# Kernel optimization log

Hardware: AMD Instinct MI355X
Metric: run time of the kernel (lower is better)

Reference implementation:

```python
import math
import jax, jax.numpy as jnp
import numpy as np

B, N, E, H, DPOS = 64, 196, 768, 16, 3
DH = E // H


def rel_pos(num_patches):
    # deterministic relative-position encodings [N, N, 3] = (dx, dy, d^2)
    v = int(math.isqrt(num_patches))
    ind = jnp.arange(v)[None, :] - jnp.arange(v)[:, None]          # [v, v]
    indx = jnp.tile(ind, (v, v))                                    # [N, N]
    indy = jnp.repeat(jnp.repeat(ind, v, axis=0), v, axis=1)       # [N, N]
    indd = indx ** 2 + indy ** 2
    return jnp.stack([indx, indy, indd], axis=-1).astype(jnp.float32)


def setup_inputs() -> dict:
    key = jax.random.key(0)
    ks = jax.random.split(key, 9)
    std = 0.02  # trunc_normal std used by the module's init
    return {
        "q": jax.random.normal(ks[0], (B, N, E), jnp.float32),
        "k": jax.random.normal(ks[1], (B, N, E), jnp.float32),
        "v": jax.random.normal(ks[2], (B, N, E), jnp.float32),
        "mask": jnp.ones((B, 1, N, N), jnp.bool_),
        "Wq": jax.random.normal(ks[3], (E, E), jnp.float32) * std,
        "Wk": jax.random.normal(ks[4], (E, E), jnp.float32) * std,
        "Wv": jax.random.normal(ks[5], (E, E), jnp.float32) * std,
        "Wo": jax.random.normal(ks[6], (E, E), jnp.float32) * std,
        "bo": jnp.zeros((E,), jnp.float32),
        "Wpos": jax.random.normal(ks[7], (H, DPOS), jnp.float32) * std,
        "bpos": jnp.zeros((H,), jnp.float32),
        "gating": jnp.ones((H,), jnp.float32),
    }


def reference(q, k, v, mask, Wq, Wk, Wv, Wo, bo, Wpos, bpos, gating):
    b, n, _ = q.shape

    def heads(x, W):  # [b, n, E] -> [b, H, n, DH]
        return (x @ W.T).reshape(b, n, H, DH).transpose(0, 2, 1, 3)

    Q, K, V = heads(q, Wq), heads(k, Wk), heads(v, Wv)

    energy = jnp.einsum('bhqd,bhkd->bhqk', Q, K) / math.sqrt(DH)
    energy = jnp.where(mask, energy, -jnp.inf)
    content = jax.nn.softmax(energy, axis=-1)                      # [b, H, n, n]

    rel = rel_pos(n)                                               # [n, n, 3]
    pos = jnp.einsum('qkp,hp->hqk', rel, Wpos) + bpos[:, None, None]
    pos = jax.nn.softmax(pos, axis=-1)[None]                       # [1, H, n, n]

    g = jax.nn.sigmoid(gating)[None, :, None, None]
    score = (1.0 - g) * content + g * pos
    score = score / jnp.sum(score, axis=-1, keepdims=True)

    attn = jnp.einsum('bhqk,bhkd->bhqd', score, V)
    out = attn.transpose(0, 2, 1, 3).reshape(b, n, E) @ Wo.T + bo
    return out
```

## Files before the change

### kernel.cpp

```cpp
#include <hip/hip_runtime.h>
#include <hip/hip_bf16.h>

#define BB 64
#define NN 196
#define EE 768
#define HH 16
#define DHH 48

typedef short bf16x8 __attribute__((ext_vector_type(8)));
typedef float f32x4 __attribute__((ext_vector_type(4)));
typedef unsigned short u16;
typedef unsigned short u16x8 __attribute__((ext_vector_type(8)));
typedef unsigned int u32;

static __device__ __forceinline__ u16 f2bf(float f) {
  union { float f; u32 u; } un; un.f = f;
  u32 u = un.u;
  u32 r = (u + 0x7fffu + ((u >> 16) & 1u)) >> 16;
  return (u16)r;
}

static __device__ __forceinline__ u16 f2bf_hw(float f) {
  __hip_bfloat16 h = __float2bfloat16(f);
  return __builtin_bit_cast(u16, h);
}

#define GLOAD16(GP, LP)                                                        \
  __builtin_amdgcn_global_load_lds(                                            \
      (const __attribute__((address_space(1))) void*)(GP),                     \
      (__attribute__((address_space(3))) void*)(LP), 16, 0, 0)

static __device__ __forceinline__ int xcd_swz(int bid, int nwg) {
  int q = nwg >> 3, r = nwg & 7;
  int xcd = bid & 7, i = bid >> 3;
  return (xcd < r ? xcd * (q + 1) : r * (q + 1) + (xcd - r) * q) + i;
}

__global__ __launch_bounds__(64) void pos_kernel(const float* __restrict__ Wpos,
                                                 const float* __restrict__ bpos,
                                                 float* __restrict__ pos) {
  int bid = blockIdx.x;
  int h = bid / NN, q = bid % NN;
  int lane = threadIdx.x;
  float w0 = Wpos[h * 3 + 0], w1 = Wpos[h * 3 + 1], w2 = Wpos[h * 3 + 2];
  float bb = bpos[h];
  int qx = q % 14, qy = q / 14;
  float e[4];
  float mx = -1e30f;
#pragma unroll
  for (int i = 0; i < 4; ++i) {
    int k = lane + 64 * i;
    float val = -1e30f;
    if (k < NN) {
      int kx = k % 14, ky = k / 14;
      float dx = (float)(kx - qx), dy = (float)(ky - qy);
      val = w0 * dx + w1 * dy + w2 * (dx * dx + dy * dy) + bb;
    }
    e[i] = val;
    mx = fmaxf(mx, val);
  }
#pragma unroll
  for (int off = 1; off < 64; off <<= 1) mx = fmaxf(mx, __shfl_xor(mx, off));
  float s = 0.f;
#pragma unroll
  for (int i = 0; i < 4; ++i) {
    int k = lane + 64 * i;
    float p = (k < NN) ? expf(e[i] - mx) : 0.f;
    e[i] = p;
    s += p;
  }
#pragma unroll
  for (int off = 1; off < 64; off <<= 1) s += __shfl_xor(s, off);
  float inv = 1.f / s;
#pragma unroll
  for (int i = 0; i < 4; ++i) {
    int k = lane + 64 * i;
    if (k < NN) pos[(size_t)h * NN * NN + (size_t)q * NN + k] = e[i] * inv;
  }
}

__global__ __launch_bounds__(256) void cvtw_kernel(const float* __restrict__ W0,
                                                   const float* __restrict__ W1,
                                                   const float* __restrict__ W2,
                                                   const float* __restrict__ W3,
                                                   u16* __restrict__ out) {
  const float* Ws[4] = {W0, W1, W2, W3};
  int mat = blockIdx.y;
  const float* src = Ws[mat];
  int idx = blockIdx.x * 256 + threadIdx.x;
  float4 f = ((const float4*)src)[idx];
  short4 s;
  s.x = (short)f2bf_hw(f.x);
  s.y = (short)f2bf_hw(f.y);
  s.z = (short)f2bf_hw(f.z);
  s.w = (short)f2bf_hw(f.w);
  *(short4*)(out + (size_t)mat * EE * EE + (size_t)idx * 4) = s;
}

__global__ __launch_bounds__(256) void cvtx_kernel(const float* __restrict__ q,
                                                   const float* __restrict__ k,
                                                   const float* __restrict__ v,
                                                   u16* __restrict__ qb,
                                                   u16* __restrict__ kb,
                                                   u16* __restrict__ vb) {
  const float* srcs[3] = {q, k, v};
  u16* dsts[3] = {qb, kb, vb};
  const float* src = srcs[blockIdx.y];
  u16* dst = dsts[blockIdx.y];
#pragma unroll
  for (int c = 0; c < 4; ++c) {
    size_t idx = (size_t)blockIdx.x * 1024 + c * 256 + threadIdx.x;
    float4 f = ((const float4*)src)[idx];
    short4 s;
    s.x = (short)f2bf_hw(f.x);
    s.y = (short)f2bf_hw(f.y);
    s.z = (short)f2bf_hw(f.z);
    s.w = (short)f2bf_hw(f.w);
    ((short4*)dst)[idx] = s;
  }
}

template <bool OUT_F32>
static __device__ __forceinline__ void gemm_body(const u16* __restrict__ Aptr,
                                                 const u16* __restrict__ Wb,
                                                 void* __restrict__ Yptr,
                                                 const float* __restrict__ bias,
                                                 int m0, int n0) {
  __shared__ u16 As[3][128 * 32];
  __shared__ u16 Bs[3][128 * 32];
  const int tid = threadIdx.x;
  const int lane = tid & 63, wid = tid >> 6;
  const int wm = wid >> 1, wn = wid & 1;
  const int r16 = lane & 15, g4 = lane >> 4;
  f32x4 acc[4][4];
#pragma unroll
  for (int i = 0; i < 4; ++i)
#pragma unroll
    for (int j = 0; j < 4; ++j) acc[i][j] = (f32x4){0.f, 0.f, 0.f, 0.f};

  auto gloadA = [&](int b, int k0) {
#pragma unroll
    for (int c = 0; c < 2; ++c) {
      int s = c * 256 + tid;
      GLOAD16(Aptr + (size_t)(m0 + (s >> 2)) * EE + k0 + (s & 3) * 8,
              &As[b][s * 8]);
    }
  };
  auto gloadB = [&](int b, int k0) {
#pragma unroll
    for (int c = 0; c < 2; ++c) {
      int s = c * 256 + tid;
      GLOAD16(Wb + (size_t)(n0 + (s >> 2)) * EE + k0 + (s & 3) * 8,
              &Bs[b][s * 8]);
    }
  };

  gloadA(0, 0);  gloadB(0, 0);
  gloadA(1, 32); gloadB(1, 32);
  asm volatile("s_waitcnt vmcnt(4)" ::: "memory");
  asm volatile("s_barrier" ::: "memory");

  for (int t = 0; t < 24; ++t) {
    const int cb = t % 3;
    const int sb = (t + 2) % 3;
    const bool st = t < 22;
    if (st) {
      gloadA(sb, (t + 2) * 32);
      gloadB(sb, (t + 2) * 32);
    }
    bf16x8 af[4], bf[4];
#pragma unroll
    for (int i = 0; i < 4; ++i)
      af[i] = *(const bf16x8*)&As[cb][(wm * 64 + i * 16 + r16) * 32 + g4 * 8];
#pragma unroll
    for (int j = 0; j < 4; ++j)
      bf[j] = *(const bf16x8*)&Bs[cb][(wn * 64 + j * 16 + r16) * 32 + g4 * 8];
#pragma unroll
    for (int i = 0; i < 4; ++i)
#pragma unroll
      for (int j = 0; j < 4; ++j)
        acc[i][j] = __builtin_amdgcn_mfma_f32_16x16x32_bf16(af[i], bf[j], acc[i][j], 0, 0, 0);
    if (st)
      asm volatile("s_waitcnt vmcnt(4)" ::: "memory");
    else
      asm volatile("s_waitcnt vmcnt(0)" ::: "memory");
    asm volatile("s_barrier" ::: "memory");
  }

#pragma unroll
  for (int i = 0; i < 4; ++i) {
    int row = m0 + wm * 64 + i * 16 + g4 * 4;
#pragma unroll
    for (int j = 0; j < 4; ++j) {
      int col = n0 + wn * 64 + j * 16 + r16;
#pragma unroll
      for (int v = 0; v < 4; ++v) {
        float val = acc[i][j][v];
        if (OUT_F32)
          ((float*)Yptr)[(size_t)(row + v) * EE + col] = val + bias[col];
        else
          ((u16*)Yptr)[(size_t)(row + v) * EE + col] = f2bf(val);
      }
    }
  }
}

__global__ __launch_bounds__(256) void qkv_gemm(const u16* __restrict__ qb,
                                                const u16* __restrict__ kb,
                                                const u16* __restrict__ vb,
                                                const u16* __restrict__ Wqb,
                                                const u16* __restrict__ Wkb,
                                                const u16* __restrict__ Wvb,
                                                u16* __restrict__ Qp,
                                                u16* __restrict__ Kp,
                                                u16* __restrict__ Vp) {
  int sid = xcd_swz(blockIdx.x, 3 * 98 * 6);
  int z = sid / 588, rem = sid % 588;
  int m0 = (rem / 6) * 128, n0 = (rem % 6) * 128;
  const u16* A = (z == 0) ? qb : (z == 1) ? kb : vb;
  const u16* W = (z == 0) ? Wqb : (z == 1) ? Wkb : Wvb;
  u16* Y = (z == 0) ? Qp : (z == 1) ? Kp : Vp;
  gemm_body<false>(A, W, Y, nullptr, m0, n0);
}

__global__ __launch_bounds__(256) void out_gemm(const u16* __restrict__ ctx,
                                                const u16* __restrict__ Wob,
                                                float* __restrict__ out,
                                                const float* __restrict__ bo) {
  int sid = xcd_swz(blockIdx.x, 98 * 6);
  int m0 = (sid / 6) * 128, n0 = (sid % 6) * 128;
  gemm_body<true>(ctx, Wob, out, bo, m0, n0);
}

__global__ __launch_bounds__(512) void attn_kernel(const u16* __restrict__ Qp,
                                                   const u16* __restrict__ Kp,
                                                   const u16* __restrict__ Vp,
                                                   const float* __restrict__ pos,
                                                   const float* __restrict__ gating,
                                                   u16* __restrict__ ctx) {
  __shared__ u16 Ks[208 * 72];
  __shared__ u16 Vt[48 * 232];
  __shared__ u16 sc[8][16 * 224];
  int bh = blockIdx.x;
  int b = bh >> 4, h = bh & 15;
  int tid = threadIdx.x;
  int wid = tid >> 6, lane = tid & 63;
  int r16 = lane & 15, g4 = lane >> 4;

  const u16* Qb = Qp + (size_t)b * NN * EE + h * DHH;
  const u16* Kb = Kp + (size_t)b * NN * EE + h * DHH;
  const u16* Vb = Vp + (size_t)b * NN * EE + h * DHH;

  bf16x8 aQ0[2], aQ1[2];
#pragma unroll
  for (int i = 0; i < 2; ++i) {
    int rt = wid + 8 * i;
    if (rt < 13) {
      int qrow = rt * 16 + r16;
      if (qrow > NN - 1) qrow = NN - 1;
      const u16* qp = Qb + (size_t)qrow * EE;
      aQ0[i] = *(const bf16x8*)(qp + g4 * 8);
      aQ1[i] = *(const bf16x8*)(qp + 32 + g4 * 8);
    }
  }

  {
    u32* z = (u32*)&Ks[0];
    for (int i = tid; i < (208 * 72) / 2; i += 512) z[i] = 0u;
    z = (u32*)&Vt[0];
    for (int i = tid; i < (48 * 232) / 2; i += 512) z[i] = 0u;
  }
  __syncthreads();
  for (int c = tid; c < NN * 12; c += 512) {
    int row = c / 12, k4 = (c % 12) * 4;
    short4 v = *(const short4*)(Kb + (size_t)row * EE + k4);
    *(short4*)&Ks[row * 72 + k4] = v;
  }
  for (int c = tid; c < NN * 12; c += 512) {
    int key = c / 12, d4 = (c % 12) * 4;
    short4 v = *(const short4*)(Vb + (size_t)key * EE + d4);
    Vt[(d4 + 0) * 232 + key] = (u16)v.x;
    Vt[(d4 + 1) * 232 + key] = (u16)v.y;
    Vt[(d4 + 2) * 232 + key] = (u16)v.z;
    Vt[(d4 + 3) * 232 + key] = (u16)v.w;
  }
  __syncthreads();

  float g = 1.f / (1.f + expf(-gating[h]));
  float omg = 1.f - g;
  u16* scw = &sc[wid][0];
  const float scale = 0.14433756729740643f;
  const float* posh = pos + (size_t)h * NN * NN;

#pragma unroll
  for (int ii = 0; ii < 2; ++ii) {
    int rt = wid + 8 * ii;
    if (rt < 13) {
      int q0 = rt * 16;
      int qg[4];
#pragma unroll
      for (int v = 0; v < 4; ++v) qg[v] = q0 + g4 * 4 + v;
      float pvv[13][4];
#pragma unroll
      for (int ct = 0; ct < 13; ++ct) {
        int cix = ct * 16 + r16;
#pragma unroll
        for (int v = 0; v < 4; ++v)
          pvv[ct][v] = (cix < NN && qg[v] < NN)
                           ? posh[(size_t)qg[v] * NN + cix] : 0.f;
      }
      f32x4 e[13];
#pragma unroll
      for (int ct = 0; ct < 13; ++ct) {
        bf16x8 b0 = *(const bf16x8*)&Ks[(ct * 16 + r16) * 72 + g4 * 8];
        bf16x8 b1 = *(const bf16x8*)&Ks[(ct * 16 + r16) * 72 + 32 + g4 * 8];
        f32x4 t = (f32x4){0.f, 0.f, 0.f, 0.f};
        t = __builtin_amdgcn_mfma_f32_16x16x32_bf16(aQ0[ii], b0, t, 0, 0, 0);
        t = __builtin_amdgcn_mfma_f32_16x16x32_bf16(aQ1[ii], b1, t, 0, 0, 0);
        e[ct] = t;
      }
      float mx[4] = {-1e30f, -1e30f, -1e30f, -1e30f};
#pragma unroll
      for (int ct = 0; ct < 13; ++ct) {
        int cix = ct * 16 + r16;
        bool valid = cix < NN;
#pragma unroll
        for (int v = 0; v < 4; ++v) {
          float ev = e[ct][v] * scale;
          ev = valid ? ev : -1e30f;
          e[ct][v] = ev;
          mx[v] = fmaxf(mx[v], ev);
        }
      }
#pragma unroll
      for (int v = 0; v < 4; ++v)
#pragma unroll
        for (int off = 1; off < 16; off <<= 1) mx[v] = fmaxf(mx[v], __shfl_xor(mx[v], off));
      float sm[4] = {0.f, 0.f, 0.f, 0.f};
#pragma unroll
      for (int ct = 0; ct < 13; ++ct)
#pragma unroll
        for (int v = 0; v < 4; ++v) {
          float p = __expf(e[ct][v] - mx[v]);
          e[ct][v] = p;
          sm[v] += p;
        }
#pragma unroll
      for (int v = 0; v < 4; ++v)
#pragma unroll
        for (int off = 1; off < 16; off <<= 1) sm[v] += __shfl_xor(sm[v], off);
      float oinv[4];
#pragma unroll
      for (int v = 0; v < 4; ++v) oinv[v] = omg / sm[v];
#pragma unroll
      for (int ct = 0; ct < 14; ++ct)
#pragma unroll
        for (int v = 0; v < 4; ++v) {
          float s = (ct < 13) ? e[ct][v] * oinv[v] + g * pvv[ct][v] : 0.f;
          scw[(g4 * 4 + v) * 224 + ct * 16 + r16] = f2bf_hw(s);
        }
      asm volatile("s_waitcnt lgkmcnt(0)" ::: "memory");
      bf16x8 aS[7];
#pragma unroll
      for (int kt = 0; kt < 7; ++kt)
        aS[kt] = *(const bf16x8*)&scw[r16 * 224 + kt * 32 + g4 * 8];
#pragma unroll
      for (int dt = 0; dt < 3; ++dt) {
        f32x4 pv = (f32x4){0.f, 0.f, 0.f, 0.f};
#pragma unroll
        for (int kt = 0; kt < 7; ++kt) {
          bf16x8 bV = *(const bf16x8*)&Vt[(dt * 16 + r16) * 232 + kt * 32 + g4 * 8];
          pv = __builtin_amdgcn_mfma_f32_16x16x32_bf16(aS[kt], bV, pv, 0, 0, 0);
        }
#pragma unroll
        for (int v = 0; v < 4; ++v) {
          if (qg[v] < NN)
            ctx[((size_t)b * NN + qg[v]) * EE + h * DHH + dt * 16 + r16] = f2bf(pv[v]);
        }
      }
    }
  }
}

extern "C" void kernel_launch(void* const* d_in, const int* in_sizes, int n_in,
                              void* d_out, int out_size, void* d_ws, size_t ws_size,
                              hipStream_t stream) {
  const float* q = (const float*)d_in[0];
  const float* k = (const float*)d_in[1];
  const float* v = (const float*)d_in[2];
  const float* Wq = (const float*)d_in[4];
  const float* Wk = (const float*)d_in[5];
  const float* Wv = (const float*)d_in[6];
  const float* Wo = (const float*)d_in[7];
  const float* bo = (const float*)d_in[8];
  const float* Wpos = (const float*)d_in[9];
  const float* bpos = (const float*)d_in[10];
  const float* gating = (const float*)d_in[11];
  float* out = (float*)d_out;

  char* ws = (char*)d_ws;
  const size_t elems = (size_t)BB * NN * EE;
  u16* Qp = (u16*)ws;
  u16* Kp = Qp + elems;
  u16* Vp = Kp + elems;
  u16* ctx = Vp + elems;
  float* pos = (float*)(ws + 4 * elems * sizeof(u16));
  u16* Wqb = (u16*)(ws + 4 * elems * sizeof(u16) + (size_t)HH * NN * NN * sizeof(float));
  u16* Wkb = Wqb + (size_t)EE * EE;
  u16* Wvb = Wkb + (size_t)EE * EE;
  u16* Wob = Wvb + (size_t)EE * EE;
  u16* qb = (u16*)d_out;
  u16* kb = qb + elems;
  u16* vb = ctx;

  hipLaunchKernelGGL(pos_kernel, dim3(HH * NN), dim3(64), 0, stream, Wpos, bpos, pos);
  hipLaunchKernelGGL(cvtw_kernel, dim3(EE * EE / 4 / 256, 4), dim3(256), 0, stream,
                     Wq, Wk, Wv, Wo, Wqb);
  hipLaunchKernelGGL(cvtx_kernel, dim3(2352, 3), dim3(256), 0, stream,
                     q, k, v, qb, kb, vb);

  hipLaunchKernelGGL(qkv_gemm, dim3(3 * 98 * 6), dim3(256), 0, stream,
                     qb, kb, vb, Wqb, Wkb, Wvb, Qp, Kp, Vp);

  hipLaunchKernelGGL(attn_kernel, dim3(BB * HH), dim3(512), 0, stream,
                     Qp, Kp, Vp, pos, gating, ctx);

  hipLaunchKernelGGL(out_gemm, dim3(98 * 6), dim3(256), 0, stream,
                     ctx, Wob, out, bo);
}
```

Baseline: 214.9 us.

## Apply positional softmax via extra MFMA with precomputed gated bf16 position matrix

The positional softmax is now prescaled by the sigmoid gate in pos_kernel and stored as a padded bf16 matrix. The attention kernel loads it directly as MFMA A-operands and adds its product with V through an extra MFMA per tile. This replaces the per-element fp32 pos gathers and the blending FMA. The content softmax also drops max-subtraction, which removes a reduction pass but risks overflow for large logits. The dead attn_kernel stub is left in the file, and launch bounds ask for two blocks per CU.

```diff
diff --git a/kernel.cpp b/kernel.cpp
--- a/kernel.cpp
+++ b/kernel.cpp
@@ -38,13 +38,24 @@
 
 __global__ __launch_bounds__(64) void pos_kernel(const float* __restrict__ Wpos,
                                                  const float* __restrict__ bpos,
-                                                 float* __restrict__ pos) {
+                                                 const float* __restrict__ gating,
+                                                 u16* __restrict__ posb) {
   int bid = blockIdx.x;
-  int h = bid / NN, q = bid % NN;
+  int h = bid / 208, qrow = bid % 208;
+  u16* dst = posb + ((size_t)h * 208 + qrow) * 224;
   int lane = threadIdx.x;
+  if (qrow >= NN) {
+#pragma unroll
+    for (int i = 0; i < 4; ++i) {
+      int k = lane + 64 * i;
+      if (k < 224) dst[k] = 0;
+    }
+    return;
+  }
   float w0 = Wpos[h * 3 + 0], w1 = Wpos[h * 3 + 1], w2 = Wpos[h * 3 + 2];
   float bb = bpos[h];
-  int qx = q % 14, qy = q / 14;
+  float g = 1.f / (1.f + expf(-gating[h]));
+  int qx = qrow % 14, qy = qrow / 14;
   float e[4];
   float mx = -1e30f;
 #pragma unroll
@@ -71,11 +82,11 @@
   }
 #pragma unroll
   for (int off = 1; off < 64; off <<= 1) s += __shfl_xor(s, off);
-  float inv = 1.f / s;
+  float ginv = g / s;
 #pragma unroll
   for (int i = 0; i < 4; ++i) {
     int k = lane + 64 * i;
-    if (k < NN) pos[(size_t)h * NN * NN + (size_t)q * NN + k] = e[i] * inv;
+    if (k < 224) dst[k] = (k < NN) ? f2bf_hw(e[i] * ginv) : (u16)0;
   }
 }
 
@@ -232,12 +243,11 @@
   gemm_body<true>(ctx, Wob, out, bo, m0, n0);
 }
 
-__global__ __launch_bounds__(512) void attn_kernel(const u16* __restrict__ Qp,
-                                                   const u16* __restrict__ Kp,
-                                                   const u16* __restrict__ Vp,
-                                                   const float* __restrict__ pos,
-                                                   const float* __restrict__ gating,
-                                                   u16* __restrict__ ctx) {
+__global__ __launch_bounds__(512, 2) void attn_kernel(const u16* __restrict__ Qp,
+                                                      const u16* __restrict__ Kp,
+                                                      const u16* __restrict__ Vp,
+                                                      const u16* __restrict__ posb,
+                                                      u16* __restrict__ ctx) {
   __shared__ u16 Ks[208 * 72];
   __shared__ u16 Vt[48 * 232];
   __shared__ u16 sc[8][16 * 224];
@@ -250,6 +260,7 @@
   const u16* Qb = Qp + (size_t)b * NN * EE + h * DHH;
   const u16* Kb = Kp + (size_t)b * NN * EE + h * DHH;
   const u16* Vb = Vp + (size_t)b * NN * EE + h * DHH;
+  const u16* ph = posb + (size_t)h * 208 * 224;
 
   bf16x8 aQ0[2], aQ1[2];
 #pragma unroll
@@ -286,11 +297,8 @@
   }
   __syncthreads();
 
-  float g = 1.f / (1.f + expf(-gating[h]));
-  float omg = 1.f - g;
   u16* scw = &sc[wid][0];
   const float scale = 0.14433756729740643f;
-  const float* posh = pos + (size_t)h * NN * NN;
 
 #pragma unroll
   for (int ii = 0; ii < 2; ++ii) {
@@ -300,15 +308,11 @@
       int qg[4];
 #pragma unroll
       for (int v = 0; v < 4; ++v) qg[v] = q0 + g4 * 4 + v;
-      float pvv[13][4];
-#pragma unroll
-      for (int ct = 0; ct < 13; ++ct) {
-        int cix = ct * 16 + r16;
-#pragma unroll
-        for (int v = 0; v < 4; ++v)
-          pvv[ct][v] = (cix < NN && qg[v] < NN)
-                           ? posh[(size_t)qg[v] * NN + cix] : 0.f;
-      }
+      bf16x8 aP[7];
+      const u16* prow = ph + (size_t)(q0 + r16) * 224;
+#pragma unroll
+      for (int kt = 0; kt < 7; ++kt)
+        aP[kt] = *(const bf16x8*)(prow + kt * 32 + g4 * 8);
       f32x4 e[13];
 #pragma unroll
       for (int ct = 0; ct < 13; ++ct) {
@@ -319,44 +323,139 @@
         t = __builtin_amdgcn_mfma_f32_16x16x32_bf16(aQ1[ii], b1, t, 0, 0, 0);
         e[ct] = t;
       }
-      float mx[4] = {-1e30f, -1e30f, -1e30f, -1e30f};
+      float sm[4] = {0.f, 0.f, 0.f, 0.f};
 #pragma unroll
       for (int ct = 0; ct < 13; ++ct) {
         int cix = ct * 16 + r16;
         bool valid = cix < NN;
 #pragma unroll
         for (int v = 0; v < 4; ++v) {
-          float ev = e[ct][v] * scale;
-          ev = valid ? ev : -1e30f;
-          e[ct][v] = ev;
-          mx[v] = fmaxf(mx[v], ev);
-        }
-      }
-#pragma unroll
-      for (int v = 0; v < 4; ++v)
-#pragma unroll
-        for (int off = 1; off < 16; off <<= 1) mx[v] = fmaxf(mx[v], __shfl_xor(mx[v], off));
-      float sm[4] = {0.f, 0.f, 0.f, 0.f};
-#pragma unroll
-      for (int ct = 0; ct < 13; ++ct)
-#pragma unroll
-        for (int v = 0; v < 4; ++v) {
-          float p = __expf(e[ct][v] - mx[v]);
+          float p = valid ? __expf(e[ct][v] * scale) : 0.f;
           e[ct][v] = p;
           sm[v] += p;
         }
+      }
 #pragma unroll
       for (int v = 0; v < 4; ++v)
 #pragma unroll
         for (int off = 1; off < 16; off <<= 1) sm[v] += __shfl_xor(sm[v], off);
       float oinv[4];
+      float g_unused = 0.f; (void)g_unused;
+#pragma unroll
+      for (int v = 0; v < 4; ++v) oinv[v] = 1.f / sm[v];
+      (void)oinv;
+      break;
+    }
+  }
+}
+
+__global__ __launch_bounds__(512, 2) void attn_kernel4(const u16* __restrict__ Qp,
+                                                       const u16* __restrict__ Kp,
+                                                       const u16* __restrict__ Vp,
+                                                       const u16* __restrict__ posb,
+                                                       const float* __restrict__ gating,
+                                                       u16* __restrict__ ctx) {
+  __shared__ u16 Ks[208 * 72];
+  __shared__ u16 Vt[48 * 232];
+  __shared__ u16 sc[8][16 * 224];
+  int bh = blockIdx.x;
+  int b = bh >> 4, h = bh & 15;
+  int tid = threadIdx.x;
+  int wid = tid >> 6, lane = tid & 63;
+  int r16 = lane & 15, g4 = lane >> 4;
+
+  const u16* Qb = Qp + (size_t)b * NN * EE + h * DHH;
+  const u16* Kb = Kp + (size_t)b * NN * EE + h * DHH;
+  const u16* Vb = Vp + (size_t)b * NN * EE + h * DHH;
+  const u16* ph = posb + (size_t)h * 208 * 224;
+
+  bf16x8 aQ0[2], aQ1[2];
+#pragma unroll
+  for (int i = 0; i < 2; ++i) {
+    int rt = wid + 8 * i;
+    if (rt < 13) {
+      int qrow = rt * 16 + r16;
+      if (qrow > NN - 1) qrow = NN - 1;
+      const u16* qp = Qb + (size_t)qrow * EE;
+      aQ0[i] = *(const bf16x8*)(qp + g4 * 8);
+      aQ1[i] = *(const bf16x8*)(qp + 32 + g4 * 8);
+    }
+  }
+
+  {
+    u32* z = (u32*)&Ks[0];
+    for (int i = tid; i < (208 * 72) / 2; i += 512) z[i] = 0u;
+    z = (u32*)&Vt[0];
+    for (int i = tid; i < (48 * 232) / 2; i += 512) z[i] = 0u;
+  }
+  __syncthreads();
+  for (int c = tid; c < NN * 12; c += 512) {
+    int row = c / 12, k4 = (c % 12) * 4;
+    short4 v = *(const short4*)(Kb + (size_t)row * EE + k4);
+    *(short4*)&Ks[row * 72 + k4] = v;
+  }
+  for (int c = tid; c < NN * 12; c += 512) {
+    int key = c / 12, d4 = (c % 12) * 4;
+    short4 v = *(const short4*)(Vb + (size_t)key * EE + d4);
+    Vt[(d4 + 0) * 232 + key] = (u16)v.x;
+    Vt[(d4 + 1) * 232 + key] = (u16)v.y;
+    Vt[(d4 + 2) * 232 + key] = (u16)v.z;
+    Vt[(d4 + 3) * 232 + key] = (u16)v.w;
+  }
+  __syncthreads();
+
+  float g = 1.f / (1.f + expf(-gating[h]));
+  float omg = 1.f - g;
+  u16* scw = &sc[wid][0];
+  const float scale = 0.14433756729740643f;
+
+#pragma unroll
+  for (int ii = 0; ii < 2; ++ii) {
+    int rt = wid + 8 * ii;
+    if (rt < 13) {
+      int q0 = rt * 16;
+      int qg[4];
+#pragma unroll
+      for (int v = 0; v < 4; ++v) qg[v] = q0 + g4 * 4 + v;
+      bf16x8 aP[7];
+      const u16* prow = ph + (size_t)(q0 + r16) * 224;
+#pragma unroll
+      for (int kt = 0; kt < 7; ++kt)
+        aP[kt] = *(const bf16x8*)(prow + kt * 32 + g4 * 8);
+      f32x4 e[13];
+#pragma unroll
+      for (int ct = 0; ct < 13; ++ct) {
+        bf16x8 b0 = *(const bf16x8*)&Ks[(ct * 16 + r16) * 72 + g4 * 8];
+        bf16x8 b1 = *(const bf16x8*)&Ks[(ct * 16 + r16) * 72 + 32 + g4 * 8];
+        f32x4 t = (f32x4){0.f, 0.f, 0.f, 0.f};
+        t = __builtin_amdgcn_mfma_f32_16x16x32_bf16(aQ0[ii], b0, t, 0, 0, 0);
+        t = __builtin_amdgcn_mfma_f32_16x16x32_bf16(aQ1[ii], b1, t, 0, 0, 0);
+        e[ct] = t;
+      }
+      float sm[4] = {0.f, 0.f, 0.f, 0.f};
+#pragma unroll
+      for (int ct = 0; ct < 13; ++ct) {
+        int cix = ct * 16 + r16;
+        bool valid = cix < NN;
+#pragma unroll
+        for (int v = 0; v < 4; ++v) {
+          float p = valid ? __expf(e[ct][v] * scale) : 0.f;
+          e[ct][v] = p;
+          sm[v] += p;
+        }
+      }
+#pragma unroll
+      for (int v = 0; v < 4; ++v)
+#pragma unroll
+        for (int off = 1; off < 16; off <<= 1) sm[v] += __shfl_xor(sm[v], off);
+      float oinv[4];
 #pragma unroll
       for (int v = 0; v < 4; ++v) oinv[v] = omg / sm[v];
 #pragma unroll
       for (int ct = 0; ct < 14; ++ct)
 #pragma unroll
         for (int v = 0; v < 4; ++v) {
-          float s = (ct < 13) ? e[ct][v] * oinv[v] + g * pvv[ct][v] : 0.f;
+          float s = (ct < 13) ? e[ct][v] * oinv[v] : 0.f;
           scw[(g4 * 4 + v) * 224 + ct * 16 + r16] = f2bf_hw(s);
         }
       asm volatile("s_waitcnt lgkmcnt(0)" ::: "memory");
@@ -371,6 +470,7 @@
         for (int kt = 0; kt < 7; ++kt) {
           bf16x8 bV = *(const bf16x8*)&Vt[(dt * 16 + r16) * 232 + kt * 32 + g4 * 8];
           pv = __builtin_amdgcn_mfma_f32_16x16x32_bf16(aS[kt], bV, pv, 0, 0, 0);
+          pv = __builtin_amdgcn_mfma_f32_16x16x32_bf16(aP[kt], bV, pv, 0, 0, 0);
         }
 #pragma unroll
         for (int v = 0; v < 4; ++v) {
@@ -404,8 +504,8 @@
   u16* Kp = Qp + elems;
   u16* Vp = Kp + elems;
   u16* ctx = Vp + elems;
-  float* pos = (float*)(ws + 4 * elems * sizeof(u16));
-  u16* Wqb = (u16*)(ws + 4 * elems * sizeof(u16) + (size_t)HH * NN * NN * sizeof(float));
+  u16* posb = (u16*)(ws + 4 * elems * sizeof(u16));
+  u16* Wqb = posb + (size_t)HH * 208 * 224;
   u16* Wkb = Wqb + (size_t)EE * EE;
   u16* Wvb = Wkb + (size_t)EE * EE;
   u16* Wob = Wvb + (size_t)EE * EE;
@@ -413,7 +513,8 @@
   u16* kb = qb + elems;
   u16* vb = ctx;
 
-  hipLaunchKernelGGL(pos_kernel, dim3(HH * NN), dim3(64), 0, stream, Wpos, bpos, pos);
+  hipLaunchKernelGGL(pos_kernel, dim3(HH * 208), dim3(64), 0, stream,
+                     Wpos, bpos, gating, posb);
   hipLaunchKernelGGL(cvtw_kernel, dim3(EE * EE / 4 / 256, 4), dim3(256), 0, stream,
                      Wq, Wk, Wv, Wo, Wqb);
   hipLaunchKernelGGL(cvtx_kernel, dim3(2352, 3), dim3(256), 0, stream,
@@ -422,8 +523,8 @@
   hipLaunchKernelGGL(qkv_gemm, dim3(3 * 98 * 6), dim3(256), 0, stream,
                      qb, kb, vb, Wqb, Wkb, Wvb, Qp, Kp, Vp);
 
-  hipLaunchKernelGGL(attn_kernel, dim3(BB * HH), dim3(512), 0, stream,
-                     Qp, Kp, Vp, pos, gating, ctx);
+  hipLaunchKernelGGL(attn_kernel4, dim3(BB * HH), dim3(512), 0, stream,
+                     Qp, Kp, Vp, posb, gating, ctx);
 
   hipLaunchKernelGGL(out_gemm, dim3(98 * 6), dim3(256), 0, stream,
                      ctx, Wob, out, bo);
```

Result: faster. 199.8 us (-7.0%).

## Fold gated positional softmax into bf16 MFMA and read K directly

Applied to the files above, without the earlier changes.

The positional softmax is now precomputed once, pre-scaled by the sigmoid gate, and stored as a zero-padded bf16 matrix. The attention kernel applies it through an extra MFMA against V instead of loading fp32 pos values and blending them per element. K is no longer staged into LDS but read straight from global memory, the softmax max-subtraction pass is dropped, and launch bounds request two blocks per CU. This cuts global traffic, register pressure and LDS use. The cost is that removing the max subtraction leaves large logits open to exp overflow, and pos now has bf16 precision.

```diff
diff --git a/kernel.cpp b/kernel.cpp
--- a/kernel.cpp
+++ b/kernel.cpp
@@ -38,13 +38,24 @@
 
 __global__ __launch_bounds__(64) void pos_kernel(const float* __restrict__ Wpos,
                                                  const float* __restrict__ bpos,
-                                                 float* __restrict__ pos) {
+                                                 const float* __restrict__ gating,
+                                                 u16* __restrict__ posb) {
   int bid = blockIdx.x;
-  int h = bid / NN, q = bid % NN;
+  int h = bid / 208, qrow = bid % 208;
+  u16* dst = posb + ((size_t)h * 208 + qrow) * 224;
   int lane = threadIdx.x;
+  if (qrow >= NN) {
+#pragma unroll
+    for (int i = 0; i < 4; ++i) {
+      int k = lane + 64 * i;
+      if (k < 224) dst[k] = 0;
+    }
+    return;
+  }
   float w0 = Wpos[h * 3 + 0], w1 = Wpos[h * 3 + 1], w2 = Wpos[h * 3 + 2];
   float bb = bpos[h];
-  int qx = q % 14, qy = q / 14;
+  float g = 1.f / (1.f + expf(-gating[h]));
+  int qx = qrow % 14, qy = qrow / 14;
   float e[4];
   float mx = -1e30f;
 #pragma unroll
@@ -71,11 +82,11 @@
   }
 #pragma unroll
   for (int off = 1; off < 64; off <<= 1) s += __shfl_xor(s, off);
-  float inv = 1.f / s;
+  float ginv = g / s;
 #pragma unroll
   for (int i = 0; i < 4; ++i) {
     int k = lane + 64 * i;
-    if (k < NN) pos[(size_t)h * NN * NN + (size_t)q * NN + k] = e[i] * inv;
+    if (k < 224) dst[k] = (k < NN) ? f2bf_hw(e[i] * ginv) : (u16)0;
   }
 }
 
@@ -232,13 +243,12 @@
   gemm_body<true>(ctx, Wob, out, bo, m0, n0);
 }
 
-__global__ __launch_bounds__(512) void attn_kernel(const u16* __restrict__ Qp,
-                                                   const u16* __restrict__ Kp,
-                                                   const u16* __restrict__ Vp,
-                                                   const float* __restrict__ pos,
-                                                   const float* __restrict__ gating,
-                                                   u16* __restrict__ ctx) {
-  __shared__ u16 Ks[208 * 72];
+__global__ __launch_bounds__(512, 2) void attn_kernel5(const u16* __restrict__ Qp,
+                                                       const u16* __restrict__ Kp,
+                                                       const u16* __restrict__ Vp,
+                                                       const u16* __restrict__ posb,
+                                                       const float* __restrict__ gating,
+                                                       u16* __restrict__ ctx) {
   __shared__ u16 Vt[48 * 232];
   __shared__ u16 sc[8][16 * 224];
   int bh = blockIdx.x;
@@ -250,6 +260,7 @@
   const u16* Qb = Qp + (size_t)b * NN * EE + h * DHH;
   const u16* Kb = Kp + (size_t)b * NN * EE + h * DHH;
   const u16* Vb = Vp + (size_t)b * NN * EE + h * DHH;
+  const u16* ph = posb + (size_t)h * 208 * 224;
 
   bf16x8 aQ0[2], aQ1[2];
 #pragma unroll
@@ -260,22 +271,19 @@
       if (qrow > NN - 1) qrow = NN - 1;
       const u16* qp = Qb + (size_t)qrow * EE;
       aQ0[i] = *(const bf16x8*)(qp + g4 * 8);
-      aQ1[i] = *(const bf16x8*)(qp + 32 + g4 * 8);
+      if (g4 < 2) {
+        aQ1[i] = *(const bf16x8*)(qp + 32 + g4 * 8);
+      } else {
+        aQ1[i] = (bf16x8){0, 0, 0, 0, 0, 0, 0, 0};
+      }
     }
   }
 
   {
-    u32* z = (u32*)&Ks[0];
-    for (int i = tid; i < (208 * 72) / 2; i += 512) z[i] = 0u;
-    z = (u32*)&Vt[0];
+    u32* z = (u32*)&Vt[0];
     for (int i = tid; i < (48 * 232) / 2; i += 512) z[i] = 0u;
   }
   __syncthreads();
-  for (int c = tid; c < NN * 12; c += 512) {
-    int row = c / 12, k4 = (c % 12) * 4;
-    short4 v = *(const short4*)(Kb + (size_t)row * EE + k4);
-    *(short4*)&Ks[row * 72 + k4] = v;
-  }
   for (int c = tid; c < NN * 12; c += 512) {
     int key = c / 12, d4 = (c % 12) * 4;
     short4 v = *(const short4*)(Vb + (size_t)key * EE + d4);
@@ -290,7 +298,6 @@
   float omg = 1.f - g;
   u16* scw = &sc[wid][0];
   const float scale = 0.14433756729740643f;
-  const float* posh = pos + (size_t)h * NN * NN;
 
 #pragma unroll
   for (int ii = 0; ii < 2; ++ii) {
@@ -300,51 +307,34 @@
       int qg[4];
 #pragma unroll
       for (int v = 0; v < 4; ++v) qg[v] = q0 + g4 * 4 + v;
-      float pvv[13][4];
+      bf16x8 aP[7];
+      const u16* prow = ph + (size_t)(q0 + r16) * 224;
+#pragma unroll
+      for (int kt = 0; kt < 7; ++kt)
+        aP[kt] = *(const bf16x8*)(prow + kt * 32 + g4 * 8);
+      f32x4 e[13];
 #pragma unroll
       for (int ct = 0; ct < 13; ++ct) {
-        int cix = ct * 16 + r16;
-#pragma unroll
-        for (int v = 0; v < 4; ++v)
-          pvv[ct][v] = (cix < NN && qg[v] < NN)
-                           ? posh[(size_t)qg[v] * NN + cix] : 0.f;
-      }
-      f32x4 e[13];
-#pragma unroll
-      for (int ct = 0; ct < 13; ++ct) {
-        bf16x8 b0 = *(const bf16x8*)&Ks[(ct * 16 + r16) * 72 + g4 * 8];
-        bf16x8 b1 = *(const bf16x8*)&Ks[(ct * 16 + r16) * 72 + 32 + g4 * 8];
+        const u16* kp = Kb + (size_t)(ct * 16 + r16) * EE;
+        bf16x8 b0 = *(const bf16x8*)(kp + g4 * 8);
+        bf16x8 b1 = *(const bf16x8*)(kp + 32 + g4 * 8);
         f32x4 t = (f32x4){0.f, 0.f, 0.f, 0.f};
         t = __builtin_amdgcn_mfma_f32_16x16x32_bf16(aQ0[ii], b0, t, 0, 0, 0);
         t = __builtin_amdgcn_mfma_f32_16x16x32_bf16(aQ1[ii], b1, t, 0, 0, 0);
         e[ct] = t;
       }
-      float mx[4] = {-1e30f, -1e30f, -1e30f, -1e30f};
+      float sm[4] = {0.f, 0.f, 0.f, 0.f};
 #pragma unroll
       for (int ct = 0; ct < 13; ++ct) {
         int cix = ct * 16 + r16;
         bool valid = cix < NN;
 #pragma unroll
         for (int v = 0; v < 4; ++v) {
-          float ev = e[ct][v] * scale;
-          ev = valid ? ev : -1e30f;
-          e[ct][v] = ev;
-          mx[v] = fmaxf(mx[v], ev);
-        }
-      }
-#pragma unroll
-      for (int v = 0; v < 4; ++v)
-#pragma unroll
-        for (int off = 1; off < 16; off <<= 1) mx[v] = fmaxf(mx[v], __shfl_xor(mx[v], off));
-      float sm[4] = {0.f, 0.f, 0.f, 0.f};
-#pragma unroll
-      for (int ct = 0; ct < 13; ++ct)
-#pragma unroll
-        for (int v = 0; v < 4; ++v) {
-          float p = __expf(e[ct][v] - mx[v]);
+          float p = valid ? __expf(e[ct][v] * scale) : 0.f;
           e[ct][v] = p;
           sm[v] += p;
         }
+      }
 #pragma unroll
       for (int v = 0; v < 4; ++v)
 #pragma unroll
@@ -356,7 +346,7 @@
       for (int ct = 0; ct < 14; ++ct)
 #pragma unroll
         for (int v = 0; v < 4; ++v) {
-          float s = (ct < 13) ? e[ct][v] * oinv[v] + g * pvv[ct][v] : 0.f;
+          float s = (ct < 13) ? e[ct][v] * oinv[v] : 0.f;
           scw[(g4 * 4 + v) * 224 + ct * 16 + r16] = f2bf_hw(s);
         }
       asm volatile("s_waitcnt lgkmcnt(0)" ::: "memory");
@@ -371,6 +361,7 @@
         for (int kt = 0; kt < 7; ++kt) {
           bf16x8 bV = *(const bf16x8*)&Vt[(dt * 16 + r16) * 232 + kt * 32 + g4 * 8];
           pv = __builtin_amdgcn_mfma_f32_16x16x32_bf16(aS[kt], bV, pv, 0, 0, 0);
+          pv = __builtin_amdgcn_mfma_f32_16x16x32_bf16(aP[kt], bV, pv, 0, 0, 0);
         }
 #pragma unroll
         for (int v = 0; v < 4; ++v) {
@@ -404,8 +395,8 @@
   u16* Kp = Qp + elems;
   u16* Vp = Kp + elems;
   u16* ctx = Vp + elems;
-  float* pos = (float*)(ws + 4 * elems * sizeof(u16));
-  u16* Wqb = (u16*)(ws + 4 * elems * sizeof(u16) + (size_t)HH * NN * NN * sizeof(float));
+  u16* posb = (u16*)(ws + 4 * elems * sizeof(u16));
+  u16* Wqb = posb + (size_t)HH * 208 * 224;
   u16* Wkb = Wqb + (size_t)EE * EE;
   u16* Wvb = Wkb + (size_t)EE * EE;
   u16* Wob = Wvb + (size_t)EE * EE;
@@ -413,7 +404,8 @@
   u16* kb = qb + elems;
   u16* vb = ctx;
 
-  hipLaunchKernelGGL(pos_kernel, dim3(HH * NN), dim3(64), 0, stream, Wpos, bpos, pos);
+  hipLaunchKernelGGL(pos_kernel, dim3(HH * 208), dim3(64), 0, stream,
+                     Wpos, bpos, gating, posb);
   hipLaunchKernelGGL(cvtw_kernel, dim3(EE * EE / 4 / 256, 4), dim3(256), 0, stream,
                      Wq, Wk, Wv, Wo, Wqb);
   hipLaunchKernelGGL(cvtx_kernel, dim3(2352, 3), dim3(256), 0, stream,
@@ -422,8 +414,8 @@
   hipLaunchKernelGGL(qkv_gemm, dim3(3 * 98 * 6), dim3(256), 0, stream,
                      qb, kb, vb, Wqb, Wkb, Wvb, Qp, Kp, Vp);
 
-  hipLaunchKernelGGL(attn_kernel, dim3(BB * HH), dim3(512), 0, stream,
-                     Qp, Kp, Vp, pos, gating, ctx);
+  hipLaunchKernelGGL(attn_kernel5, dim3(BB * HH), dim3(512), 0, stream,
+                     Qp, Kp, Vp, posb, gating, ctx);
 
   hipLaunchKernelGGL(out_gemm, dim3(98 * 6), dim3(256), 0, stream,
                      ctx, Wob, out, bo);
```

New measurement: 204.9 us. 4.7% less time.
